# Optimization experiments

Hardware: AMD Instinct MI355X
Metric: run time of the kernel (lower is better)

Reference implementation:

```python
import jax, jax.numpy as jnp
import numpy as np

B, S, D = 4, 2048, 1024
HALF_PI = np.float32(np.pi / 2.0)


def setup_inputs() -> dict:
    key = jax.random.key(0)
    ks = jax.random.split(key, 12)
    std = np.float32(0.02)
    def w(k):
        return jax.random.normal(k, (D, D), dtype=jnp.float32) * std
    return {
        "x": jax.random.normal(ks[0], (B, S, D), dtype=jnp.float32),
        "W_q": w(ks[1]), "b_q": jnp.zeros((D,), jnp.float32),
        "W_k": w(ks[2]), "b_k": jnp.zeros((D,), jnp.float32),
        "W_v": w(ks[3]), "b_v": jnp.zeros((D,), jnp.float32),
        "W_t": w(ks[4]), "b_t": jnp.zeros((D,), jnp.float32),
        "W_o": w(ks[5]), "b_o": jnp.zeros((D,), jnp.float32),
        "entangle_strength": jnp.float32(0.5),
    }


def reference(x, W_q, b_q, W_k, b_k, W_v, b_v, W_t, b_t, W_o, b_o, entangle_strength):
    scale = jnp.float32(np.sqrt(D))
    Q = x @ W_q + b_q          # [B,S,D]
    K = x @ W_k + b_k
    V = x @ W_v + b_v
    # theta in [0, pi/2]; r = cos(2*theta)
    theta_q = jax.nn.sigmoid(Q @ W_t + b_t) * HALF_PI
    theta_k = jax.nn.sigmoid(K @ W_t + b_t) * HALF_PI
    r_q = jnp.cos(2.0 * theta_q)
    r_k = jnp.cos(2.0 * theta_k)
    classical = jnp.einsum("bqd,bkd->bqk", Q, K) / scale
    quantum = jnp.einsum("bqd,bkd->bqk", r_q, r_k) * entangle_strength
    attn_weights = jax.nn.softmax(classical + quantum, axis=-1)  # [B,S,S]
    # dropout: eval mode -> identity
    out = jnp.einsum("bqk,bkd->bqd", attn_weights, V)
    out = out @ W_o + b_o
    return out, attn_weights
```

## Files before the change

kernel.cpp:

```cpp
#include <hip/hip_runtime.h>
#include <cstdint>

typedef unsigned short u16;
typedef __attribute__((ext_vector_type(8))) short bf16x8;
typedef __attribute__((ext_vector_type(4))) float f32x4;

__device__ __forceinline__ u16 f2b(float x) {
  unsigned u = __float_as_uint(x);
  u += 0x7FFFu + ((u >> 16) & 1u);
  return (u16)(u >> 16);
}

__device__ __forceinline__ void gload16(const void* g, void* l) {
  __builtin_amdgcn_global_load_lds(
      (const __attribute__((address_space(1))) void*)g,
      (__attribute__((address_space(3))) void*)l, 16, 0, 0);
}

template <int N>
__device__ __forceinline__ void vmwait() {
  if constexpr (N == 0) asm volatile("s_waitcnt vmcnt(0)" ::: "memory");
  else if constexpr (N == 4) asm volatile("s_waitcnt vmcnt(4)" ::: "memory");
  else if constexpr (N == 6) asm volatile("s_waitcnt vmcnt(6)" ::: "memory");
}

__device__ __forceinline__ void stage128(const u16* __restrict__ G,
                                         long long ld, int kb,
                                         u16* Ldst, int tid) {
#pragma unroll
  for (int j = 0; j < 2; ++j) {
    const int P = j * 256 + tid;
    const int vr = P >> 3;
    const int ch = (P & 7) ^ (vr & 7);
    const int r = vr * 2 + (ch >> 2), c = ch & 3;
    gload16(G + (long long)r * ld + kb + c * 8, Ldst + P * 8);
  }
}

__device__ __forceinline__ bf16x8 fr4(const u16* R, int row, int chunk) {
  const int vr = row >> 1;
  const int ch = (((row & 1) << 2) | chunk) ^ (vr & 7);
  return *(const bf16x8*)(R + vr * 64 + ch * 8);
}

__device__ __forceinline__ void swz_xcd(int hw, int S, int gx,
                                        int& bx, int& by) {
  const int l = (hw & 7) * (S >> 3) + (hw >> 3);
  bx = l % gx;
  by = l / gx;
}

template <int EPI>
__device__ __forceinline__ void gemm_core(
    u16* lds, int bx, int by, int z,
    const u16* __restrict__ A, long long lda, long long sAz,
    const u16* __restrict__ B, long long ldb, long long sBz,
    void* __restrict__ C0, void* __restrict__ C1,
    long long ldc, long long sCz, int K,
    const float* __restrict__ b0, const float* __restrict__ b1,
    float preScale, const float* __restrict__ esp) {
  constexpr int HALF = 4096;
  constexpr int BUFU = 2 * HALF;
  const long long tM = (long long)by * 128;
  const long long tN = (long long)bx * 128;
  const u16* GA = A + z * sAz + tM * lda;
  const u16* GB = B + z * sBz + tN * ldb;
  const int tid = threadIdx.x;
  const int NT = K >> 5;

  stage128(GA, lda, 0, lds, tid);
  stage128(GB, ldb, 0, lds + HALF, tid);
  stage128(GA, lda, 32, lds + BUFU, tid);
  stage128(GB, ldb, 32, lds + BUFU + HALF, tid);

  const int wid = tid >> 6, lane = tid & 63;
  const int wr = (wid >> 1) * 64, wc = (wid & 1) * 64;
  const int lr = lane & 15, cA = lane >> 4;
  f32x4 acc[4][4] = {};

  for (int t = 0; t < NT; ++t) {
    if (t < NT - 1) vmwait<4>(); else vmwait<0>();
    __builtin_amdgcn_s_barrier();
    if (t + 2 < NT) {
      u16* nxt = lds + ((t + 2) % 3) * BUFU;
      stage128(GA, lda, (t + 2) * 32, nxt, tid);
      stage128(GB, ldb, (t + 2) * 32, nxt + HALF, tid);
    }
    const u16* cur = lds + (t % 3) * BUFU;
    bf16x8 a[4], b[4];
#pragma unroll
    for (int m = 0; m < 4; ++m) a[m] = fr4(cur, wr + m * 16 + lr, cA);
#pragma unroll
    for (int n = 0; n < 4; ++n) b[n] = fr4(cur + HALF, wc + n * 16 + lr, cA);
#pragma unroll
    for (int m = 0; m < 4; ++m)
#pragma unroll
      for (int n = 0; n < 4; ++n)
        acc[m][n] = __builtin_amdgcn_mfma_f32_16x16x32_bf16(a[m], b[n],
                                                            acc[m][n], 0, 0, 0);
  }

  const int rr = (lane >> 4) << 2;
  float ps = preScale, mul = 1.0f;
  if constexpr (EPI == 1) {
    ps = (z == 0) ? preScale : 1.0f;
    mul = (z == 0) ? esp[0] : 1.0f;
  }
#pragma unroll
  for (int m = 0; m < 4; ++m) {
#pragma unroll
    for (int n = 0; n < 4; ++n) {
      const int col = (int)tN + wc + n * 16 + lr;
#pragma unroll
      for (int r = 0; r < 4; ++r) {
        const long long row = tM + wr + m * 16 + rr + r;
        const float v = acc[m][n][r];
        if constexpr (EPI == 0) {
          const int g = col >> 10, cc = col & 1023;
          if (g == 0) ((u16*)C0)[row * 2048 + cc] = f2b((v + b0[cc]) * 0.03125f);
          else        ((u16*)C1)[row * 2048 + cc] = f2b(v + b1[cc]);
        } else if constexpr (EPI == 1) {
          const float tt = v * ps + b0[col];
          const float sg = 1.f / (1.f + __expf(-tt));
          ((u16*)C0)[z * sCz + row * ldc + col] = f2b(mul * cospif(sg));
        } else if constexpr (EPI == 2) {
          ((u16*)C0)[z * sCz + row * ldc + col] = f2b(v);
        } else if constexpr (EPI == 3) {
          ((float*)C0)[z * sCz + row * ldc + col] = v + b0[col];
        } else {
          ((float*)C0)[z * sCz + row * ldc + col] = v;
        }
      }
    }
  }
}

template <int EPI>
__device__ __forceinline__ void wide_core(
    u16* lds, int bx, int by, int z,
    const u16* __restrict__ A, long long lda, long long sAz,
    const u16* __restrict__ B, long long ldb, long long sBz,
    void* __restrict__ C0, void* __restrict__ C1,
    long long ldc, long long sCz, int K,
    const float* __restrict__ b0, const float* __restrict__ b1,
    float preScale, const float* __restrict__ esp) {
  constexpr int AS = 4096;
  constexpr int BUFU = AS + 8192;
  const long long tM = (long long)by * 128;
  const long long tN = (long long)bx * 256;
  const u16* GA = A + z * sAz + tM * lda;
  const u16* GB = B + z * sBz + tN * ldb;
  const int tid = threadIdx.x;
  const int NT = K >> 5;

#define STAGE_W(kb, buf)                                         \
  do {                                                           \
    stage128(GA, lda, (kb), (buf), tid);                         \
    stage128(GB, ldb, (kb), (buf) + AS, tid);                    \
    stage128(GB + 128 * ldb, ldb, (kb), (buf) + AS + 4096, tid); \
  } while (0)

  STAGE_W(0, lds);
  STAGE_W(32, lds + BUFU);

  const int wid = tid >> 6, lane = tid & 63;
  const int wr = (wid >> 1) * 64, wc = (wid & 1) * 128;
  const int lr = lane & 15, cA = lane >> 4;
  f32x4 acc[4][8] = {};

  for (int t = 0; t < NT; ++t) {
    if (t < NT - 1) vmwait<6>(); else vmwait<0>();
    __builtin_amdgcn_s_barrier();
    if (t + 2 < NT) STAGE_W((t + 2) * 32, lds + ((t + 2) % 3) * BUFU);
    const u16* cur = lds + (t % 3) * BUFU;
    const u16* Bs = cur + AS + (wid & 1) * 4096;
    bf16x8 a[4], b[8];
#pragma unroll
    for (int m = 0; m < 4; ++m) a[m] = fr4(cur, wr + m * 16 + lr, cA);
#pragma unroll
    for (int n = 0; n < 8; ++n) b[n] = fr4(Bs, n * 16 + lr, cA);
#pragma unroll
    for (int m = 0; m < 4; ++m)
#pragma unroll
      for (int n = 0; n < 8; ++n)
        acc[m][n] = __builtin_amdgcn_mfma_f32_16x16x32_bf16(a[m], b[n],
                                                            acc[m][n], 0, 0, 0);
  }
#undef STAGE_W

  const int rr = (lane >> 4) << 2;
  float ps = preScale, mul = 1.0f;
  if constexpr (EPI == 1) {
    ps = (z == 0) ? preScale : 1.0f;
    mul = (z == 0) ? esp[0] : 1.0f;
  }
#pragma unroll
  for (int m = 0; m < 4; ++m) {
#pragma unroll
    for (int n = 0; n < 8; ++n) {
      const int col = (int)tN + wc + n * 16 + lr;
#pragma unroll
      for (int r = 0; r < 4; ++r) {
        const long long row = tM + wr + m * 16 + rr + r;
        const float v = acc[m][n][r];
        if constexpr (EPI == 0) {
          const int g = col >> 10, cc = col & 1023;
          if (g == 0) ((u16*)C0)[row * 2048 + cc] = f2b((v + b0[cc]) * 0.03125f);
          else        ((u16*)C1)[row * 2048 + cc] = f2b(v + b1[cc]);
        } else if constexpr (EPI == 1) {
          const float tt = v * ps + b0[col];
          const float sg = 1.f / (1.f + __expf(-tt));
          ((u16*)C0)[z * sCz + row * ldc + col] = f2b(mul * cospif(sg));
        } else if constexpr (EPI == 2) {
          ((u16*)C0)[z * sCz + row * ldc + col] = f2b(v);
        } else {
          ((float*)C0)[z * sCz + row * ldc + col] = v;
        }
      }
    }
  }
}

__global__ __launch_bounds__(256, 2) void e3s(
    const u16* __restrict__ A, long long lda, long long sAz,
    const u16* __restrict__ B, long long ldb, long long sBz,
    float* __restrict__ C, long long ldc, long long sCz, int K) {
  __shared__ __align__(16) u16 lds[3 * 12288];
  int bx, by;
  swz_xcd(blockIdx.y * gridDim.x + blockIdx.x, gridDim.x * gridDim.y,
          gridDim.x, bx, by);
  wide_core<4>(lds, bx, by, blockIdx.z, A, lda, sAz, B, ldb, sBz,
               C, nullptr, ldc, sCz, K, nullptr, nullptr, 1.f, nullptr);
}

template <int EPI>
__global__ __launch_bounds__(256, 3) void e3p(
    const u16* __restrict__ A, long long lda, long long sAz,
    const u16* __restrict__ B, long long ldb, long long sBz,
    void* __restrict__ C0, long long ldc, long long sCz, int K,
    const float* __restrict__ b0) {
  __shared__ __align__(16) u16 lds[3 * 8192];
  int bx, by;
  swz_xcd(blockIdx.y * gridDim.x + blockIdx.x, gridDim.x * gridDim.y,
          gridDim.x, bx, by);
  gemm_core<EPI>(lds, bx, by, blockIdx.z, A, lda, sAz, B, ldb, sBz,
                 C0, nullptr, ldc, sCz, K, b0, nullptr, 1.f, nullptr);
}

__global__ __launch_bounds__(256, 3) void qk_wvo(
    const u16* __restrict__ XB, u16* __restrict__ WT,
    u16* __restrict__ Qc, u16* __restrict__ Kc,
    const float* __restrict__ bq, const float* __restrict__ bk) {
  __shared__ __align__(16) u16 lds[3 * 8192];
  const int id = blockIdx.x;
  if (id < 1024) {
    int bx, by;
    swz_xcd(id, 1024, 16, bx, by);
    gemm_core<0>(lds, bx, by, 0, XB, 1024, 0, WT, 1024, 0,
                 Qc, Kc, 2048, 0, 1024, bq, bk, 1.f, nullptr);
  } else {
    int bx, by;
    swz_xcd(id - 1024, 64, 8, bx, by);
    gemm_core<2>(lds, bx, by, 0, WT + (3LL << 20), 1024, 0,
                 WT + (4LL << 20), 1024, 0, WT + (5LL << 20), nullptr,
                 1024, 0, 1024, nullptr, nullptr, 1.f, nullptr);
  }
}

__global__ __launch_bounds__(256, 2) void theta_xvt(
    u16* __restrict__ Qcat, const u16* __restrict__ WT,
    const u16* __restrict__ XB, u16* __restrict__ XVT_,
    const float* __restrict__ bt, const float* __restrict__ esp) {
  __shared__ __align__(16) u16 lds[3 * 12288];
  const int id = blockIdx.x;
  if (id < 512) {
    const int z = id >> 8;
    int bx, by;
    swz_xcd(id & 255, 256, 4, bx, by);
    wide_core<1>(lds, bx, by, z, Qcat, 2048, 16777216LL,
                 WT + (2LL << 20), 1024, 0, Qcat + 1024, nullptr,
                 2048, 16777216LL, 1024, bt, nullptr, 32.f, esp);
  } else {
    const int e = id - 512, z = e >> 7;
    int bx, by;
    swz_xcd(e & 127, 128, 16, bx, by);
    gemm_core<2>(lds, bx, by, z, WT + (5LL << 20), 1024, 0,
                 XB, 1024, 2097152LL, XVT_, nullptr,
                 2048, 2097152LL, 1024, nullptr, nullptr, 1.f, nullptr);
  }
}

__global__ __launch_bounds__(256) void prep_all(
    const float* __restrict__ x,
    const float* __restrict__ Wq, const float* __restrict__ Wk,
    const float* __restrict__ Wt, const float* __restrict__ Wo,
    const float* __restrict__ Wv, const float* __restrict__ bv,
    const float* __restrict__ bo,
    u16* __restrict__ XB, u16* __restrict__ WT, float* __restrict__ BF) {
  __shared__ float sh[32][33];
  const int id = blockIdx.x;
  const int thr = threadIdx.x;
  if (id < 8192) {
    const int i = id * 256 + thr;
    float4 v = ((const float4*)x)[i];
    ((ushort4*)XB)[i] = make_ushort4(f2b(v.x), f2b(v.y), f2b(v.z), f2b(v.w));
  } else if (id < 13312) {
    const int w = id - 8192;
    const int z = w >> 10, rem = w & 1023;
    const int cx = rem & 31, cy = rem >> 5;
    const float* W = (z == 0) ? Wq : (z == 1) ? Wk : (z == 2) ? Wt
                   : (z == 3) ? Wo : Wv;
    u16* D = WT + ((long long)z << 20);
    const int c0 = cx * 32, r0 = cy * 32;
    const int tx = thr & 31, ty = thr >> 5;
    if (z == 4) {
#pragma unroll
      for (int i = 0; i < 4; ++i) {
        const long long idx = (long long)(r0 + ty + i * 8) * 1024 + c0 + tx;
        D[idx] = f2b(W[idx]);
      }
      return;
    }
#pragma unroll
    for (int i = 0; i < 4; ++i)
      sh[ty + i * 8][tx] = W[(long long)(r0 + ty + i * 8) * 1024 + c0 + tx];
    __syncthreads();
#pragma unroll
    for (int i = 0; i < 4; ++i)
      D[(long long)(c0 + ty + i * 8) * 1024 + r0 + tx] = f2b(sh[tx][ty + i * 8]);
  } else {
    const int i = id - 13312;
    float acc = 0.f;
    for (int k = thr; k < 1024; k += 256)
      acc += bv[k] * Wo[(long long)k * 1024 + i];
    float* red = &sh[0][0];
    red[thr] = acc;
    __syncthreads();
    for (int s = 128; s > 0; s >>= 1) {
      if (thr < s) red[thr] += red[thr + s];
      __syncthreads();
    }
    if (thr == 0) BF[i] = red[0] + bo[i];
  }
}

__global__ __launch_bounds__(256) void softmax_rows(float* __restrict__ L,
                                                    u16* __restrict__ AB) {
  const long long row = blockIdx.x;
  float4* p4 = (float4*)(L + row * 2048);
  const int tid = threadIdx.x;
  float4 a = p4[tid], b = p4[tid + 256];
  float m = fmaxf(fmaxf(fmaxf(a.x, a.y), fmaxf(a.z, a.w)),
                  fmaxf(fmaxf(b.x, b.y), fmaxf(b.z, b.w)));
#pragma unroll
  for (int o = 32; o > 0; o >>= 1) m = fmaxf(m, __shfl_xor(m, o));
  __shared__ float rmax[4], rsum[4];
  const int wid = tid >> 6, lane = tid & 63;
  if (lane == 0) rmax[wid] = m;
  __syncthreads();
  m = fmaxf(fmaxf(rmax[0], rmax[1]), fmaxf(rmax[2], rmax[3]));
  a.x = __expf(a.x - m); a.y = __expf(a.y - m);
  a.z = __expf(a.z - m); a.w = __expf(a.w - m);
  b.x = __expf(b.x - m); b.y = __expf(b.y - m);
  b.z = __expf(b.z - m); b.w = __expf(b.w - m);
  float s = a.x + a.y + a.z + a.w + b.x + b.y + b.z + b.w;
#pragma unroll
  for (int o = 32; o > 0; o >>= 1) s += __shfl_xor(s, o);
  if (lane == 0) rsum[wid] = s;
  __syncthreads();
  s = rsum[0] + rsum[1] + rsum[2] + rsum[3];
  const float inv = 1.0f / s;
  a.x *= inv; a.y *= inv; a.z *= inv; a.w *= inv;
  b.x *= inv; b.y *= inv; b.z *= inv; b.w *= inv;
  p4[tid] = a;
  p4[tid + 256] = b;
  ushort4* o4 = (ushort4*)(AB + row * 2048);
  o4[tid]       = make_ushort4(f2b(a.x), f2b(a.y), f2b(a.z), f2b(a.w));
  o4[tid + 256] = make_ushort4(f2b(b.x), f2b(b.y), f2b(b.z), f2b(b.w));
}

extern "C" void kernel_launch(void* const* d_in, const int* in_sizes, int n_in,
                              void* d_out, int out_size, void* d_ws,
                              size_t ws_size, hipStream_t stream) {
  const float* x  = (const float*)d_in[0];
  const float* Wq = (const float*)d_in[1];
  const float* bq = (const float*)d_in[2];
  const float* Wk = (const float*)d_in[3];
  const float* bk = (const float*)d_in[4];
  const float* Wv = (const float*)d_in[5];
  const float* bv = (const float*)d_in[6];
  const float* Wt = (const float*)d_in[7];
  const float* bt = (const float*)d_in[8];
  const float* Wo = (const float*)d_in[9];
  const float* bo = (const float*)d_in[10];
  const float* es = (const float*)d_in[11];

  char* ws = (char*)d_ws;
  u16* WT    = (u16*)(ws);
  float* BF  = (float*)(ws + 12582912);
  u16* XB    = (u16*)(ws + 12587008);
  u16* Qcat  = (u16*)(ws + 29364224);
  u16* Kcat  = Qcat + 16777216;
  u16* XVT   = (u16*)(ws + 96473088);
  u16* ATT   = Qcat;

  float* outO = (float*)d_out;
  float* outA = outO + 8388608;

  prep_all<<<14336, 256, 0, stream>>>(x, Wq, Wk, Wt, Wo, Wv, bv, bo,
                                      XB, WT, BF);
  qk_wvo<<<1088, 256, 0, stream>>>(XB, WT, Qcat, Kcat, bq, bk);
  theta_xvt<<<1024, 256, 0, stream>>>(Qcat, WT, XB, XVT, bt, es);
  e3s<<<dim3(8, 16, 4), 256, 0, stream>>>(
      Qcat, 2048, 4194304, Kcat, 2048, 4194304,
      outA, 2048, 4194304, 2048);
  softmax_rows<<<8192, 256, 0, stream>>>(outA, ATT);
  e3p<3><<<dim3(8, 16, 4), 256, 0, stream>>>(
      ATT, 2048, 4194304, XVT, 2048, 2097152,
      outO, 1024, 2097152, 2048, BF);
}
```

Baseline: 308.6 us.

## Switch theta GEMM to smaller tiles and interleave with XVT blocks

The theta projection moves from the wide 128x256 tile core to the standard gemm_core with a smaller tile, doubling its block count. Theta and XVT blocks are interleaved 2:1 in block order so the two workloads share the GPU concurrently rather than running back to back. LDS is shrunk and launch bounds raised to 3 blocks per CU to increase occupancy. The wide core epilogue is reduced to the plain float store, since only e3s still uses it. The smaller tile costs some operand reuse per block.

```diff
diff --git a/kernel.cpp b/kernel.cpp
--- a/kernel.cpp
+++ b/kernel.cpp
@@ -189,11 +189,6 @@
 #undef STAGE_W
 
   const int rr = (lane >> 4) << 2;
-  float ps = preScale, mul = 1.0f;
-  if constexpr (EPI == 1) {
-    ps = (z == 0) ? preScale : 1.0f;
-    mul = (z == 0) ? esp[0] : 1.0f;
-  }
 #pragma unroll
   for (int m = 0; m < 4; ++m) {
 #pragma unroll
@@ -202,20 +197,7 @@
 #pragma unroll
       for (int r = 0; r < 4; ++r) {
         const long long row = tM + wr + m * 16 + rr + r;
-        const float v = acc[m][n][r];
-        if constexpr (EPI == 0) {
-          const int g = col >> 10, cc = col & 1023;
-          if (g == 0) ((u16*)C0)[row * 2048 + cc] = f2b((v + b0[cc]) * 0.03125f);
-          else        ((u16*)C1)[row * 2048 + cc] = f2b(v + b1[cc]);
-        } else if constexpr (EPI == 1) {
-          const float tt = v * ps + b0[col];
-          const float sg = 1.f / (1.f + __expf(-tt));
-          ((u16*)C0)[z * sCz + row * ldc + col] = f2b(mul * cospif(sg));
-        } else if constexpr (EPI == 2) {
-          ((u16*)C0)[z * sCz + row * ldc + col] = f2b(v);
-        } else {
-          ((float*)C0)[z * sCz + row * ldc + col] = v;
-        }
+        ((float*)C0)[z * sCz + row * ldc + col] = acc[m][n][r];
       }
     }
   }
@@ -267,21 +249,24 @@
   }
 }
 
-__global__ __launch_bounds__(256, 2) void theta_xvt(
+__global__ __launch_bounds__(256, 3) void theta_xvt(
     u16* __restrict__ Qcat, const u16* __restrict__ WT,
     const u16* __restrict__ XB, u16* __restrict__ XVT_,
     const float* __restrict__ bt, const float* __restrict__ esp) {
-  __shared__ __align__(16) u16 lds[3 * 12288];
+  __shared__ __align__(16) u16 lds[3 * 8192];
   const int id = blockIdx.x;
-  if (id < 512) {
-    const int z = id >> 8;
+  const int trip = id / 3, rem = id - trip * 3;
+  if (rem < 2) {
+    const int tix = trip * 2 + rem;
+    const int z = tix >> 9;
     int bx, by;
-    swz_xcd(id & 255, 256, 4, bx, by);
-    wide_core<1>(lds, bx, by, z, Qcat, 2048, 16777216LL,
+    swz_xcd(tix & 511, 512, 8, bx, by);
+    gemm_core<1>(lds, bx, by, z, Qcat, 2048, 16777216LL,
                  WT + (2LL << 20), 1024, 0, Qcat + 1024, nullptr,
                  2048, 16777216LL, 1024, bt, nullptr, 32.f, esp);
   } else {
-    const int e = id - 512, z = e >> 7;
+    const int e = trip;
+    const int z = e >> 7;
     int bx, by;
     swz_xcd(e & 127, 128, 16, bx, by);
     gemm_core<2>(lds, bx, by, z, WT + (5LL << 20), 1024, 0,
@@ -410,7 +395,7 @@
   prep_all<<<14336, 256, 0, stream>>>(x, Wq, Wk, Wt, Wo, Wv, bv, bo,
                                       XB, WT, BF);
   qk_wvo<<<1088, 256, 0, stream>>>(XB, WT, Qcat, Kcat, bq, bk);
-  theta_xvt<<<1024, 256, 0, stream>>>(Qcat, WT, XB, XVT, bt, es);
+  theta_xvt<<<1536, 256, 0, stream>>>(Qcat, WT, XB, XVT, bt, es);
   e3s<<<dim3(8, 16, 4), 256, 0, stream>>>(
       Qcat, 2048, 4194304, Kcat, 2048, 4194304,
       outA, 2048, 4194304, 2048);
```

New measurement: 311.3 us. Within noise of the previous version (+0.9%).
